# Kernel tuning notes

Measured on AMD Instinct MI355X. Metric: run time of the kernel, lower is better.

The kernel has to match this reference:

```python
import jax, jax.numpy as jnp
import numpy as np

KNN_K = 5          # neighbor count hard-coded in the original forward (get_entropy(..., k=5))
SAMPLE_K = 256     # self.k: number of tokens sampled per batch item
EPS = 1e-12


def _knn_entropy(x):
    """Per-point k-NN entropy weight: distance to the KNN_K-th nearest neighbor.

    x: [B, N, D] -> [B, N] nonnegative weights (Kozachenko-Leonenko style; the
    per-point entropy contribution is monotone in log d_k, and multinomial
    weights must be nonnegative, so we use d_k itself as the weight).
    """
    B, N, D = x.shape
    sq = jnp.sum(x * x, axis=-1)                                   # [B, N]
    d2 = sq[:, :, None] + sq[:, None, :] - 2.0 * jnp.einsum('bnd,bmd->bnm', x, x)  # [B,N,N]
    d2 = jnp.maximum(d2, 0.0)
    idx = jnp.arange(N)
    d2 = d2.at[:, idx, idx].set(jnp.inf)                           # exclude self
    neg_smallest, _ = jax.lax.top_k(-d2, KNN_K)                    # [B, N, KNN_K]
    dk2 = -neg_smallest[..., -1]                                   # sq dist to k-th NN
    return jnp.sqrt(dk2 + EPS)                                     # [B, N]


def setup_inputs() -> dict:
    key = jax.random.key(0)
    x = jax.random.normal(key, (8, 4096, 256), dtype=jnp.float32)
    return {"x": x}


def reference(x):
    # entropy weights per token (batched; replaces the per-batch numpy loop)
    w = _knn_entropy(x)                                            # [B, N]
    # multinomial sampling WITHOUT replacement via Gumbel top-k trick
    key = jax.random.key(42)
    g = jax.random.gumbel(key, w.shape, dtype=w.dtype)             # [B, N]
    scores = jnp.log(w + EPS) + g
    _, sampled_idx = jax.lax.top_k(scores, SAMPLE_K)               # [B, SAMPLE_K]
    # gather sampled tokens
    sampled = jnp.take_along_axis(x, sampled_idx[:, :, None], axis=1)  # [B, SAMPLE_K, D]
    return (sampled, 0.0)
```

## Files before the change

### kernel.cpp

```cpp
#include <hip/hip_runtime.h>
#include <math.h>
#include <stdint.h>

#define BATCH 8
#define NTOK  4096
#define DIM   256
#define SK    256
#define BQ    128
#define BM    128
#define BK    64
#define MH    2048
#define TOPK  10
#define CANDH 44

typedef __attribute__((ext_vector_type(8))) _Float16 half8;
typedef __attribute__((ext_vector_type(4))) float float4v;
typedef __attribute__((ext_vector_type(16))) float f32x16;

#define GLOAD_LDS16(gp, lp)                                                    \
  __builtin_amdgcn_global_load_lds(                                            \
      (const __attribute__((address_space(1))) unsigned int*)(gp),             \
      (__attribute__((address_space(3))) unsigned int*)(lp), 16, 0, 0)

__device__ __forceinline__ uint32_t umin32(uint32_t a, uint32_t b) { return a < b ? a : b; }
__device__ __forceinline__ uint32_t umax32(uint32_t a, uint32_t b) { return a > b ? a : b; }

__device__ __forceinline__ uint32_t rotl32(uint32_t v, uint32_t r) {
  return (v << r) | (v >> (32u - r));
}
__device__ __forceinline__ void tf_round4(uint32_t& x0, uint32_t& x1,
                                          uint32_t r0, uint32_t r1,
                                          uint32_t r2, uint32_t r3) {
  x0 += x1; x1 = rotl32(x1, r0); x1 ^= x0;
  x0 += x1; x1 = rotl32(x1, r1); x1 ^= x0;
  x0 += x1; x1 = rotl32(x1, r2); x1 ^= x0;
  x0 += x1; x1 = rotl32(x1, r3); x1 ^= x0;
}
__device__ __forceinline__ uint32_t threefry_bits32(uint32_t c_hi, uint32_t c_lo) {
  const uint32_t k0 = 0u, k1 = 42u;
  const uint32_t k2 = k0 ^ k1 ^ 0x1BD11BDAu;
  uint32_t x0 = c_hi + k0;
  uint32_t x1 = c_lo + k1;
  tf_round4(x0, x1, 13u, 15u, 26u, 6u);  x0 += k1; x1 += k2 + 1u;
  tf_round4(x0, x1, 17u, 29u, 16u, 24u); x0 += k2; x1 += k0 + 2u;
  tf_round4(x0, x1, 13u, 15u, 26u, 6u);  x0 += k0; x1 += k1 + 3u;
  tf_round4(x0, x1, 17u, 29u, 16u, 24u); x0 += k1; x1 += k2 + 4u;
  tf_round4(x0, x1, 13u, 15u, 26u, 6u);  x0 += k2; x1 += k0 + 5u;
  return x0 ^ x1;
}

__global__ __launch_bounds__(256) void tofp16_rowsq_kernel(
    const float* __restrict__ x, unsigned short* __restrict__ xh,
    float* __restrict__ sqf) {
  const int row  = blockIdx.x * 4 + (threadIdx.x >> 6);
  const int lane = threadIdx.x & 63;
  const float* xr = x + (size_t)row * DIM;
  double acc = 0.0;
#pragma unroll
  for (int i = 0; i < 4; ++i) {
    const float v = xr[lane + i * 64];
    const _Float16 h = (_Float16)v;
    xh[(size_t)row * DIM + lane + i * 64] = *(const unsigned short*)&h;
    acc += (double)v * (double)v;
  }
#pragma unroll
  for (int off = 32; off > 0; off >>= 1) acc += __shfl_down(acc, off, 64);
  if (lane == 0) sqf[row] = (float)acc;
}

__global__ __launch_bounds__(256, 2) void gemm_knn_kernel(
    const unsigned short* __restrict__ xh, const float* __restrict__ sqf,
    int* __restrict__ cand) {
  __shared__ union {
    unsigned short Bf[2][8192];
    uint32_t M[512][10];
  } U;

  const int wid = (blockIdx.x & 7) * 64 + (blockIdx.x >> 3);
  const int b   = wid >> 6;
  const int qt  = (wid >> 1) & 31;
  const int mh  = wid & 1;
  const int q0  = qt * BQ;
  const int mbase = mh * MH;
  const int t  = threadIdx.x;
  const int w  = t >> 6;
  const int l  = t & 63;
  const int l5 = l & 31;
  const int hi2 = l >> 5;

  const unsigned short* xhb = xh + (size_t)b * NTOK * DIM;
  const float* sqb = sqf + b * NTOK;

  auto stageB = [&](int buf, int m0s, int kb) {
    const int m = m0s + w * 32 + l5;
    const unsigned short* src = xhb + (size_t)m * DIM + kb + hi2 * 8;
#pragma unroll
    for (int c = 0; c < 4; ++c) {
      GLOAD_LDS16(src + c * 16,
                  (char*)&U.Bf[0][0] + buf * 16384 + (c * 4 + w) * 1024 + l * 16);
    }
  };
  stageB(0, mbase, 0);

  const int qg = q0 + w * 32 + l5;
  const unsigned short* qrow = xhb + (size_t)qg * DIM;
  half8 af[16];
#pragma unroll
  for (int kk = 0; kk < 16; ++kk)
    af[kk] = *(const half8*)(qrow + kk * 16 + hi2 * 8);
  const float sqq = sqb[qg];

  __syncthreads();

  uint32_t tv0[TOPK], tv1[TOPK];
#pragma unroll
  for (int j = 0; j < TOPK; ++j) { tv0[j] = 0xFFFFFFFFu; tv1[j] = 0xFFFFFFFFu; }

  for (int mt = 0; mt < MH / BM; ++mt) {
    const int m0 = mbase + mt * BM;
    f32x16 acc[4];
#pragma unroll
    for (int ii = 0; ii < 4; ++ii) acc[ii] = (f32x16)(0.0f);

#pragma unroll
    for (int ks = 0; ks < 4; ++ks) {
      const int s = mt * 4 + ks;
      const int buf = s & 1;
      if (s + 1 < (MH / BM) * 4) {
        const int sn = s + 1;
        stageB(buf ^ 1, mbase + (sn >> 2) * BM, (sn & 3) * BK);
      }
#pragma unroll
      for (int kap = 0; kap < 4; ++kap) {
        const int kk = ks * 4 + kap;
#pragma unroll
        for (int ii = 0; ii < 4; ++ii) {
          const half8 mf = *(const half8*)((const char*)&U.Bf[0][0] +
                                           buf * 16384 + (kap * 4 + ii) * 1024 + l * 16);
          acc[ii] = __builtin_amdgcn_mfma_f32_32x32x16_f16(mf, af[kk], acc[ii], 0, 0, 0);
        }
      }
      __syncthreads();
    }

#pragma unroll
    for (int ii = 0; ii < 4; ++ii) {
      const int mb = m0 + ii * 32 + hi2 * 4;
#pragma unroll
      for (int c = 0; c < 4; ++c) {
        const float4v sqm = *(const float4v*)(sqb + mb + c * 8);
        uint32_t* tv = (c < 2) ? tv0 : tv1;
#pragma unroll
        for (int r = 0; r < 4; ++r) {
          const int mg = mb + c * 8 + r;
          const float d2a = sqq + sqm[r] - 2.0f * acc[ii][c * 4 + r];
          const uint32_t u = (__float_as_uint(d2a) & 0xFFFFF000u) | (uint32_t)mg;
          if (u < tv[TOPK - 1]) {
            uint32_t v = u;
#pragma unroll
            for (int k2 = 0; k2 < TOPK; ++k2) {
              const uint32_t lo = umin32(tv[k2], v);
              v = umax32(tv[k2], v);
              tv[k2] = lo;
            }
          }
        }
      }
    }
  }

  __syncthreads();
  {
    const int base = ((w * 32 + l5) << 2) + (hi2 << 1);
#pragma unroll
    for (int j = 0; j < TOPK; ++j) { U.M[base][j] = tv0[j]; U.M[base + 1][j] = tv1[j]; }
  }
  __syncthreads();
  if (t < BQ) {
    const int q = t;
    const int qglob = q0 + q;
    const int kidx = ((qglob >> 11) == mh) ? 5 : 4;
    uint32_t t6[6];
#pragma unroll
    for (int j = 0; j < 6; ++j) t6[j] = 0xFFFFFFFFu;
    for (int s = 0; s < 4; ++s)
      for (int j = 0; j < 6; ++j) {
        const uint32_t v = U.M[q * 4 + s][j];
        if (v < t6[5]) {
          uint32_t vv = v;
#pragma unroll
          for (int k2 = 0; k2 < 6; ++k2) {
            const uint32_t lo = umin32(t6[k2], vv);
            vv = umax32(t6[k2], vv);
            t6[k2] = lo;
          }
        }
      }
    const float T = __uint_as_float(t6[kidx] & 0xFFFFF000u) + 2.0f;
    int cnt = 0, ov = 0;
    int* cq = cand + (size_t)(b * NTOK + qglob) * (2 * CANDH) + mh * CANDH;
    for (int s = 0; s < 4; ++s) {
      const uint32_t last = U.M[q * 4 + s][TOPK - 1];
      if (__uint_as_float(last & 0xFFFFF000u) < T) ov = 1;
      for (int j = 0; j < TOPK; ++j) {
        const uint32_t v = U.M[q * 4 + s][j];
        if (__uint_as_float(v & 0xFFFFF000u) <= T && cnt < 4 * TOPK)
          cq[1 + cnt++] = (int)(v & 0xFFFu);
      }
    }
    cq[0] = ov ? -1 : cnt;
  }
}

__global__ __launch_bounds__(256) void exact_knn_score_kernel(
    const float* __restrict__ x, const int* __restrict__ cand,
    double* __restrict__ scores) {
  const int qg = blockIdx.x * 4 + (threadIdx.x >> 6);
  const int l  = threadIdx.x & 63;
  const int b  = qg >> 12;
  const int q  = qg & (NTOK - 1);
  const float* xb = x + (size_t)b * NTOK * DIM;
  const int* cq = cand + (size_t)qg * (2 * CANDH);

  double xq[4];
#pragma unroll
  for (int i = 0; i < 4; ++i) xq[i] = (double)xb[(size_t)q * DIM + l + i * 64];

  double t5[5] = {1e300, 1e300, 1e300, 1e300, 1e300};
  auto process = [&](int m) {
    double acc = 0.0;
#pragma unroll
    for (int i = 0; i < 4; ++i) {
      const double d = xq[i] - (double)xb[(size_t)m * DIM + l + i * 64];
      acc += d * d;
    }
#pragma unroll
    for (int off = 32; off > 0; off >>= 1) acc += __shfl_xor(acc, off, 64);
    if (acc < t5[4]) {
      t5[4] = acc;
#pragma unroll
      for (int k2 = 4; k2 > 0; --k2)
        if (t5[k2] < t5[k2 - 1]) { double tmp = t5[k2]; t5[k2] = t5[k2 - 1]; t5[k2 - 1] = tmp; }
    }
  };

  for (int h = 0; h < 2; ++h) {
    const int cnt = cq[h * CANDH];
    if (cnt >= 0) {
      for (int c = 0; c < cnt; ++c) {
        const int m = cq[h * CANDH + 1 + c];
        if (m == q) continue;
        process(m);
      }
    } else {
      const int mb = h * MH;
      for (int m = mb; m < mb + MH; ++m) {
        if (m == q) continue;
        process(m);
      }
    }
  }

  if (l == 0) {
    const uint32_t bits = threefry_bits32(0u, (uint32_t)qg);
    const uint32_t fb = (bits >> 9) | 0x3F800000u;
    float uf = __uint_as_float(fb) - 1.0f;
    const float tiny = 1.17549435082228750797e-38f;
    uf += tiny;
    if (uf < tiny) uf = tiny;
    const double g = -log(-log((double)uf));
    const double wv = sqrt(t5[4] + 1e-12);
    scores[qg] = log(wv + 1e-12) + g;
  }
}

__global__ __launch_bounds__(1024) void sort_topk_kernel(
    const double* __restrict__ scores, int* __restrict__ sel) {
  __shared__ unsigned long long ko[NTOK];
  __shared__ int ki[NTOK];
  const int b = blockIdx.x;
  const int t = threadIdx.x;
  for (int i = t; i < NTOK; i += 1024) {
    const double s = scores[(size_t)b * NTOK + i];
    unsigned long long u = (unsigned long long)__double_as_longlong(s);
    u = (u & 0x8000000000000000ull) ? ~u : (u | 0x8000000000000000ull);
    ko[i] = u; ki[i] = i;
  }
  __syncthreads();
  for (int k = 2; k <= NTOK; k <<= 1) {
    for (int j = k >> 1; j > 0; j >>= 1) {
      for (int base = 0; base < NTOK; base += 1024) {
        const int i = base + t;
        const int p = i ^ j;
        if (p > i) {
          const bool up = (i & k) == 0;
          unsigned long long a = ko[i], c = ko[p];
          int ia = ki[i], ic = ki[p];
          const bool p_beats = (c > a) || (c == a && ic < ia);
          const bool i_beats = (a > c) || (a == c && ia < ic);
          const bool sw = up ? p_beats : i_beats;
          if (sw) { ko[i] = c; ko[p] = a; ki[i] = ic; ki[p] = ia; }
        }
      }
      __syncthreads();
    }
  }
  if (t < SK) sel[b * SK + t] = ki[t];
}

__global__ __launch_bounds__(256) void gather_kernel(const float* __restrict__ x,
                                                     const int* __restrict__ sel,
                                                     float* __restrict__ out) {
  const int blk = blockIdx.x;
  const int b = blk >> 8;
  const int r = blk & 255;
  const int t = threadIdx.x;
  const int src = sel[b * SK + r];
  out[((size_t)(b * SK + r)) * DIM + t] = x[((size_t)(b * NTOK + src)) * DIM + t];
  if (blk == 0 && t == 0) out[(size_t)BATCH * SK * DIM] = 0.0f;
}

extern "C" void kernel_launch(void* const* d_in, const int* in_sizes, int n_in,
                              void* d_out, int out_size, void* d_ws, size_t ws_size,
                              hipStream_t stream) {
  const float* x = (const float*)d_in[0];
  float* out = (float*)d_out;
  char* ws = (char*)d_ws;

  double* scores  = (double*)(ws + 0);
  float*  sqf     = (float*)(ws + 262144);
  int*    sel     = (int*)(ws + 393216);
  unsigned short* xh = (unsigned short*)(ws + 1048576);
  int*    cand    = (int*)(ws + 17825792);

  tofp16_rowsq_kernel<<<BATCH * NTOK / 4, 256, 0, stream>>>(x, xh, sqf);
  gemm_knn_kernel<<<BATCH * (NTOK / BQ) * 2, 256, 0, stream>>>(xh, sqf, cand);
  exact_knn_score_kernel<<<BATCH * NTOK / 4, 256, 0, stream>>>(x, cand, scores);
  sort_topk_kernel<<<BATCH, 1024, 0, stream>>>(scores, sel);
  gather_kernel<<<BATCH * SK, 256, 0, stream>>>(x, sel, out);
}
```

Baseline: 448.3 us.

## Split key range into quarters and use branchless top-k insertion

The GEMM-kNN kernel now splits the key dimension into four 1024-token quarters instead of two halves. This doubles the grid to 1024 blocks for better occupancy and load balance, and halves the serial work per block. The candidate buffer layout and the exact-scoring kernel are updated to consume four candidate segments per query. The per-element top-10 insertion is made branchless, which avoids divergence at the cost of always running the compare-swap network. The exact kernel now evaluates more candidates and writes more candidate data.

Result: slower. 499.3 us (+11.4%).

```diff
diff --git a/kernel.cpp b/kernel.cpp
--- a/kernel.cpp
+++ b/kernel.cpp
@@ -9,9 +9,9 @@
 #define BQ    128
 #define BM    128
 #define BK    64
-#define MH    2048
+#define MQ    1024
 #define TOPK  10
-#define CANDH 44
+#define CANDQ 44
 
 typedef __attribute__((ext_vector_type(8))) _Float16 half8;
 typedef __attribute__((ext_vector_type(4))) float float4v;
@@ -76,12 +76,12 @@
     uint32_t M[512][10];
   } U;
 
-  const int wid = (blockIdx.x & 7) * 64 + (blockIdx.x >> 3);
-  const int b   = wid >> 6;
-  const int qt  = (wid >> 1) & 31;
-  const int mh  = wid & 1;
+  const int wid = (blockIdx.x & 7) * 128 + (blockIdx.x >> 3);
+  const int b   = wid >> 7;
+  const int qt  = (wid >> 2) & 31;
+  const int mq  = wid & 3;
   const int q0  = qt * BQ;
-  const int mbase = mh * MH;
+  const int mbase = mq * MQ;
   const int t  = threadIdx.x;
   const int w  = t >> 6;
   const int l  = t & 63;
@@ -116,7 +116,7 @@
 #pragma unroll
   for (int j = 0; j < TOPK; ++j) { tv0[j] = 0xFFFFFFFFu; tv1[j] = 0xFFFFFFFFu; }
 
-  for (int mt = 0; mt < MH / BM; ++mt) {
+  for (int mt = 0; mt < MQ / BM; ++mt) {
     const int m0 = mbase + mt * BM;
     f32x16 acc[4];
 #pragma unroll
@@ -126,7 +126,7 @@
     for (int ks = 0; ks < 4; ++ks) {
       const int s = mt * 4 + ks;
       const int buf = s & 1;
-      if (s + 1 < (MH / BM) * 4) {
+      if (s + 1 < (MQ / BM) * 4) {
         const int sn = s + 1;
         stageB(buf ^ 1, mbase + (sn >> 2) * BM, (sn & 3) * BK);
       }
@@ -154,15 +154,12 @@
         for (int r = 0; r < 4; ++r) {
           const int mg = mb + c * 8 + r;
           const float d2a = sqq + sqm[r] - 2.0f * acc[ii][c * 4 + r];
-          const uint32_t u = (__float_as_uint(d2a) & 0xFFFFF000u) | (uint32_t)mg;
-          if (u < tv[TOPK - 1]) {
-            uint32_t v = u;
-#pragma unroll
-            for (int k2 = 0; k2 < TOPK; ++k2) {
-              const uint32_t lo = umin32(tv[k2], v);
-              v = umax32(tv[k2], v);
-              tv[k2] = lo;
-            }
+          uint32_t v = (__float_as_uint(d2a) & 0xFFFFF000u) | (uint32_t)mg;
+#pragma unroll
+          for (int k2 = 0; k2 < TOPK; ++k2) {
+            const uint32_t lo = umin32(tv[k2], v);
+            v = umax32(tv[k2], v);
+            tv[k2] = lo;
           }
         }
       }
@@ -179,7 +176,7 @@
   if (t < BQ) {
     const int q = t;
     const int qglob = q0 + q;
-    const int kidx = ((qglob >> 11) == mh) ? 5 : 4;
+    const int kidx = ((qglob >> 10) == mq) ? 5 : 4;
     uint32_t t6[6];
 #pragma unroll
     for (int j = 0; j < 6; ++j) t6[j] = 0xFFFFFFFFu;
@@ -198,7 +195,7 @@
       }
     const float T = __uint_as_float(t6[kidx] & 0xFFFFF000u) + 2.0f;
     int cnt = 0, ov = 0;
-    int* cq = cand + (size_t)(b * NTOK + qglob) * (2 * CANDH) + mh * CANDH;
+    int* cq = cand + (size_t)(b * NTOK + qglob) * (4 * CANDQ) + mq * CANDQ;
     for (int s = 0; s < 4; ++s) {
       const uint32_t last = U.M[q * 4 + s][TOPK - 1];
       if (__uint_as_float(last & 0xFFFFF000u) < T) ov = 1;
@@ -220,7 +217,7 @@
   const int b  = qg >> 12;
   const int q  = qg & (NTOK - 1);
   const float* xb = x + (size_t)b * NTOK * DIM;
-  const int* cq = cand + (size_t)qg * (2 * CANDH);
+  const int* cq = cand + (size_t)qg * (4 * CANDQ);
 
   double xq[4];
 #pragma unroll
@@ -244,17 +241,17 @@
     }
   };
 
-  for (int h = 0; h < 2; ++h) {
-    const int cnt = cq[h * CANDH];
+  for (int h = 0; h < 4; ++h) {
+    const int cnt = cq[h * CANDQ];
     if (cnt >= 0) {
       for (int c = 0; c < cnt; ++c) {
-        const int m = cq[h * CANDH + 1 + c];
+        const int m = cq[h * CANDQ + 1 + c];
         if (m == q) continue;
         process(m);
       }
     } else {
-      const int mb = h * MH;
-      for (int m = mb; m < mb + MH; ++m) {
+      const int mb = h * MQ;
+      for (int m = mb; m < mb + MQ; ++m) {
         if (m == q) continue;
         process(m);
       }
@@ -334,7 +331,7 @@
   int*    cand    = (int*)(ws + 17825792);
 
   tofp16_rowsq_kernel<<<BATCH * NTOK / 4, 256, 0, stream>>>(x, xh, sqf);
-  gemm_knn_kernel<<<BATCH * (NTOK / BQ) * 2, 256, 0, stream>>>(xh, sqf, cand);
+  gemm_knn_kernel<<<BATCH * 32 * 4, 256, 0, stream>>>(xh, sqf, cand);
   exact_knn_score_kernel<<<BATCH * NTOK / 4, 256, 0, stream>>>(x, cand, scores);
   sort_topk_kernel<<<BATCH, 1024, 0, stream>>>(scores, sel);
   gather_kernel<<<BATCH * SK, 256, 0, stream>>>(x, sel, out);
```
